# Kernel tuning notes

Hardware: AMD Instinct MI355X
Metric: run time of the kernel (lower is better)

## Reference

```python
import jax, jax.numpy as jnp
import numpy as np
from jax import lax

M = 4194304      # total ray samples
N_RAYS = 16384   # number of rays
INTERVAL = 0.5
ALPHA_INIT = 1e-6


def setup_inputs() -> dict:
    key = jax.random.key(0)
    k1, k2, k3 = jax.random.split(key, 3)
    density = jax.random.normal(k1, (M,), dtype=jnp.float32)
    rgb_raw = jax.random.normal(k2, (M, 3), dtype=jnp.float32)
    # act_shift buffer: log(1/(1-alpha_init) - 1)
    shift = jnp.full((1,), np.log(1.0 / (1.0 - ALPHA_INIT) - 1.0), dtype=jnp.float32)
    ray_id = jnp.sort(jax.random.randint(k3, (M,), 0, N_RAYS, dtype=jnp.int32))
    return {"density": density, "rgb_raw": rgb_raw, "shift": shift,
            "ray_id": ray_id, "N": N_RAYS}


def _seg_comb(a, b):
    # associative operator for segmented product scan: (prod, reset_flag)
    pa, fa = a
    pb, fb = b
    return jnp.where(fb, pb, pa * pb), fa | fb


def reference(density, rgb_raw, shift, ray_id, N):
    # Raw2Alpha: alpha = 1 - exp(-softplus(density + shift) * interval)
    s = jax.nn.softplus(density + shift[0]) * INTERVAL   # [M], >= 0
    alpha = -jnp.expm1(-s)                                # 1 - exp(-s), stable
    om = jnp.exp(-s)                                      # 1 - alpha, exact

    # Alphas2Weights: per-ray transmittance scan over variable-length segments.
    first = jnp.concatenate([jnp.ones((1,), bool), ray_id[1:] != ray_id[:-1]])
    # inclusive segmented cumprod of (1 - alpha)
    Tin, _ = lax.associative_scan(_seg_comb, (om, first))
    # exclusive transmittance: T_i = prod of (1-alpha_j) for j earlier in same ray
    T = jnp.where(first, 1.0, jnp.concatenate([jnp.ones((1,), om.dtype), Tin[:-1]]))
    weights = alpha * T                                   # [M]
    # leftover transmittance per ray (1 for rays with no samples)
    alphainv_last = jax.ops.segment_prod(om, ray_id, num_segments=N)  # [N]

    # alpha compositing of colors against a white background
    rgb = jax.nn.sigmoid(rgb_raw)                          # [M,3]
    rgb_marched = (jax.ops.segment_sum(weights[:, None] * rgb, ray_id, num_segments=N)
                   + alphainv_last[:, None])               # [N,3]
    return rgb_marched
```

## Files before the change

### kernel.cpp

```cpp
#include <hip/hip_runtime.h>
#include <math.h>


__device__ __forceinline__ float sigm(float x) {
    return __builtin_amdgcn_rcpf(1.0f + __expf(-x));
}

template <int Ctrl, int RowMask>
__device__ __forceinline__ float dpp_mul(float x) {
    const int s = __builtin_amdgcn_update_dpp(
        __float_as_int(1.0f), __float_as_int(x), Ctrl, RowMask, 0xf, false);
    return x * __int_as_float(s);
}
template <int Ctrl, int RowMask>
__device__ __forceinline__ float dpp_add(float x) {
    const int s = __builtin_amdgcn_update_dpp(
        __float_as_int(0.0f), __float_as_int(x), Ctrl, RowMask, 0xf, false);
    return x + __int_as_float(s);
}

__device__ __forceinline__ float wave_cumprod(float p) {
    p = dpp_mul<0x111, 0xf>(p);
    p = dpp_mul<0x112, 0xf>(p);
    p = dpp_mul<0x114, 0xf>(p);
    p = dpp_mul<0x118, 0xf>(p);
    p = dpp_mul<0x142, 0xa>(p);
    p = dpp_mul<0x143, 0xc>(p);
    return p;
}
__device__ __forceinline__ float wave_cumsum(float a) {
    a = dpp_add<0x111, 0xf>(a);
    a = dpp_add<0x112, 0xf>(a);
    a = dpp_add<0x114, 0xf>(a);
    a = dpp_add<0x118, 0xf>(a);
    a = dpp_add<0x142, 0xa>(a);
    a = dpp_add<0x143, 0xc>(a);
    return a;
}
__device__ __forceinline__ float lane63(float x) {
    return __int_as_float(__builtin_amdgcn_readlane(__float_as_int(x), 63));
}

__global__ __launch_bounds__(256) void seg_starts_kernel(
    const int* __restrict__ ray_id, int* __restrict__ starts, int M, int N)
{
    const int i4 = (blockIdx.x * 256 + threadIdx.x) * 4;
    if (i4 >= M) return;

    if (i4 + 3 < M) {
        const int4 v = *(const int4*)(ray_id + i4);
        const int prev = (i4 == 0) ? -1 : ray_id[i4 - 1];
        for (int r = prev + 1; r <= v.x; ++r) starts[r] = i4 + 0;
        for (int r = v.x + 1; r <= v.y; ++r) starts[r] = i4 + 1;
        for (int r = v.y + 1; r <= v.z; ++r) starts[r] = i4 + 2;
        for (int r = v.z + 1; r <= v.w; ++r) starts[r] = i4 + 3;
        if (i4 + 4 == M) {
            for (int r = v.w + 1; r <= N; ++r) starts[r] = M;
        }
    } else {
        int prev = (i4 == 0) ? -1 : ray_id[i4 - 1];
        for (int k = 0; k < 4 && i4 + k < M; ++k) {
            const int cur = ray_id[i4 + k];
            for (int r = prev + 1; r <= cur; ++r) starts[r] = i4 + k;
            prev = cur;
            if (i4 + k == M - 1)
                for (int r = cur + 1; r <= N; ++r) starts[r] = M;
        }
    }
}

__global__ __launch_bounds__(256) void voxel_march_kernel(
    const float* __restrict__ density,
    const float* __restrict__ rgb_raw,
    const float* __restrict__ shift,
    const int*   __restrict__ starts,
    float* __restrict__ out,
    int M, int N)
{
    const int lane = threadIdx.x & 63;
    const int wave = threadIdx.x >> 6;
    const int ray  = blockIdx.x * 4 + wave;
    if (ray >= N) return;

    const float sh = shift[0];
    const int begin = starts[ray];
    const int end   = starts[ray + 1];

    float carry = 1.0f;
    float acc0 = 0.0f, acc1 = 0.0f, acc2 = 0.0f;

    for (int base = (begin & ~3); base < end; base += 256) {
        const int b4 = base + 4 * lane;
        const int ba = min(b4, M - 4);

        const float4 dd = *(const float4*)(density + ba);
        const float4* rp = (const float4*)(rgb_raw + 3 * ba);
        const float4 c0 = rp[0], c1 = rp[1], c2 = rp[2];

        const bool v0 = (b4 + 0 >= begin) & (b4 + 0 < end);
        const bool v1 = (b4 + 1 >= begin) & (b4 + 1 < end);
        const bool v2 = (b4 + 2 >= begin) & (b4 + 2 < end);
        const bool v3 = (b4 + 3 >= begin) & (b4 + 3 < end);
        const float d0 = v0 ? dd.x : -1e30f;
        const float d1 = v1 ? dd.y : -1e30f;
        const float d2 = v2 ? dd.z : -1e30f;
        const float d3 = v3 ? dd.w : -1e30f;

        const float om0 = __builtin_amdgcn_rsqf(1.0f + __expf(d0 + sh));
        const float om1 = __builtin_amdgcn_rsqf(1.0f + __expf(d1 + sh));
        const float om2 = __builtin_amdgcn_rsqf(1.0f + __expf(d2 + sh));
        const float om3 = __builtin_amdgcn_rsqf(1.0f + __expf(d3 + sh));
        const float al0 = 1.0f - om0, al1 = 1.0f - om1;
        const float al2 = 1.0f - om2, al3 = 1.0f - om3;

        const float p = wave_cumprod((om0 * om1) * (om2 * om3));

        const float excl = __int_as_float(__builtin_amdgcn_update_dpp(
            __float_as_int(1.0f), __float_as_int(p), 0x138, 0xf, 0xf, false));

        float t = carry * excl;
        const float w0 = al0 * t; t *= om0;
        const float w1 = al1 * t; t *= om1;
        const float w2 = al2 * t; t *= om2;
        const float w3 = al3 * t;

        acc0 += w0 * sigm(c0.x) + w1 * sigm(c0.w) + w2 * sigm(c1.z) + w3 * sigm(c2.y);
        acc1 += w0 * sigm(c0.y) + w1 * sigm(c1.x) + w2 * sigm(c1.w) + w3 * sigm(c2.z);
        acc2 += w0 * sigm(c0.z) + w1 * sigm(c1.y) + w2 * sigm(c2.x) + w3 * sigm(c2.w);

        carry *= lane63(p);
    }

    const float tot0 = lane63(wave_cumsum(acc0));
    const float tot1 = lane63(wave_cumsum(acc1));
    const float tot2 = lane63(wave_cumsum(acc2));

    if (lane == 0) {
        out[3 * ray + 0] = tot0 + carry;
        out[3 * ray + 1] = tot1 + carry;
        out[3 * ray + 2] = tot2 + carry;
    }
}

extern "C" void kernel_launch(void* const* d_in, const int* in_sizes, int n_in,
                              void* d_out, int out_size, void* d_ws, size_t ws_size,
                              hipStream_t stream)
{
    const float* density = (const float*)d_in[0];
    const float* rgb_raw = (const float*)d_in[1];
    const float* shift   = (const float*)d_in[2];
    const int*   ray_id  = (const int*)d_in[3];
    float* out = (float*)d_out;

    const int M = in_sizes[0];
    const int N = out_size / 3;

    int* starts = (int*)d_ws;
    const int t1 = (M + 3) / 4;
    seg_starts_kernel<<<(t1 + 255) / 256, 256, 0, stream>>>(ray_id, starts, M, N);

    const int rays_per_block = 4;
    const int blocks = (N + rays_per_block - 1) / rays_per_block;
    voxel_march_kernel<<<blocks, 256, 0, stream>>>(density, rgb_raw, shift,
                                                   starts, out, M, N);
}
```

Before: 111.1 us.

## Replace per-ray marching with dense chunked segmented scan plus stitch pass

```diff
diff --git a/kernel.cpp b/kernel.cpp
--- a/kernel.cpp
+++ b/kernel.cpp
@@ -2,144 +2,198 @@
 #include <math.h>
 
 
+#define CHUNK 256
+
 __device__ __forceinline__ float sigm(float x) {
     return __builtin_amdgcn_rcpf(1.0f + __expf(-x));
 }
 
 template <int Ctrl, int RowMask>
-__device__ __forceinline__ float dpp_mul(float x) {
-    const int s = __builtin_amdgcn_update_dpp(
-        __float_as_int(1.0f), __float_as_int(x), Ctrl, RowMask, 0xf, false);
-    return x * __int_as_float(s);
+__device__ __forceinline__ float dpp_movf(float x, float old) {
+    return __int_as_float(__builtin_amdgcn_update_dpp(
+        __float_as_int(old), __float_as_int(x), Ctrl, RowMask, 0xf, false));
 }
 template <int Ctrl, int RowMask>
-__device__ __forceinline__ float dpp_add(float x) {
-    const int s = __builtin_amdgcn_update_dpp(
-        __float_as_int(0.0f), __float_as_int(x), Ctrl, RowMask, 0xf, false);
-    return x + __int_as_float(s);
-}
-
-__device__ __forceinline__ float wave_cumprod(float p) {
-    p = dpp_mul<0x111, 0xf>(p);
-    p = dpp_mul<0x112, 0xf>(p);
-    p = dpp_mul<0x114, 0xf>(p);
-    p = dpp_mul<0x118, 0xf>(p);
-    p = dpp_mul<0x142, 0xa>(p);
-    p = dpp_mul<0x143, 0xc>(p);
-    return p;
-}
-__device__ __forceinline__ float wave_cumsum(float a) {
-    a = dpp_add<0x111, 0xf>(a);
-    a = dpp_add<0x112, 0xf>(a);
-    a = dpp_add<0x114, 0xf>(a);
-    a = dpp_add<0x118, 0xf>(a);
-    a = dpp_add<0x142, 0xa>(a);
-    a = dpp_add<0x143, 0xc>(a);
-    return a;
-}
-__device__ __forceinline__ float lane63(float x) {
-    return __int_as_float(__builtin_amdgcn_readlane(__float_as_int(x), 63));
-}
-
-__global__ __launch_bounds__(256) void seg_starts_kernel(
-    const int* __restrict__ ray_id, int* __restrict__ starts, int M, int N)
-{
-    const int i4 = (blockIdx.x * 256 + threadIdx.x) * 4;
-    if (i4 >= M) return;
-
-    if (i4 + 3 < M) {
-        const int4 v = *(const int4*)(ray_id + i4);
-        const int prev = (i4 == 0) ? -1 : ray_id[i4 - 1];
-        for (int r = prev + 1; r <= v.x; ++r) starts[r] = i4 + 0;
-        for (int r = v.x + 1; r <= v.y; ++r) starts[r] = i4 + 1;
-        for (int r = v.y + 1; r <= v.z; ++r) starts[r] = i4 + 2;
-        for (int r = v.z + 1; r <= v.w; ++r) starts[r] = i4 + 3;
-        if (i4 + 4 == M) {
-            for (int r = v.w + 1; r <= N; ++r) starts[r] = M;
-        }
-    } else {
-        int prev = (i4 == 0) ? -1 : ray_id[i4 - 1];
-        for (int k = 0; k < 4 && i4 + k < M; ++k) {
-            const int cur = ray_id[i4 + k];
-            for (int r = prev + 1; r <= cur; ++r) starts[r] = i4 + k;
-            prev = cur;
-            if (i4 + k == M - 1)
-                for (int r = cur + 1; r <= N; ++r) starts[r] = M;
-        }
-    }
-}
-
-__global__ __launch_bounds__(256) void voxel_march_kernel(
+__device__ __forceinline__ int dpp_movi(int x, int old) {
+    return __builtin_amdgcn_update_dpp(old, x, Ctrl, RowMask, 0xf, false);
+}
+
+struct Seg { float p, s0, s1, s2; int f; };
+
+template <int Ctrl, int RowMask>
+__device__ __forceinline__ void seg_step(Seg& a) {
+    const float pp = dpp_movf<Ctrl, RowMask>(a.p, 1.0f);
+    const float t0 = dpp_movf<Ctrl, RowMask>(a.s0, 0.0f);
+    const float t1 = dpp_movf<Ctrl, RowMask>(a.s1, 0.0f);
+    const float t2 = dpp_movf<Ctrl, RowMask>(a.s2, 0.0f);
+    const int   ff = dpp_movi<Ctrl, RowMask>(a.f, 0);
+    const bool cut = (a.f != 0);
+    const float pa = cut ? 1.0f : pp;
+    a.s0 = fmaf(pa, a.s0, cut ? 0.0f : t0);
+    a.s1 = fmaf(pa, a.s1, cut ? 0.0f : t1);
+    a.s2 = fmaf(pa, a.s2, cut ? 0.0f : t2);
+    a.p  = pa * a.p;
+    a.f  = a.f | ff;
+}
+
+__global__ __launch_bounds__(256) void march_dense_kernel(
     const float* __restrict__ density,
     const float* __restrict__ rgb_raw,
     const float* __restrict__ shift,
-    const int*   __restrict__ starts,
+    const int*   __restrict__ ray_id,
     float* __restrict__ out,
-    int M, int N)
+    int2*   __restrict__ ids,
+    float4* __restrict__ head,
+    float4* __restrict__ tail,
+    int C)
 {
     const int lane = threadIdx.x & 63;
     const int wave = threadIdx.x >> 6;
-    const int ray  = blockIdx.x * 4 + wave;
-    if (ray >= N) return;
+    const int c    = blockIdx.x * 4 + wave;
+    if (c >= C) return;
+    const int base = c * CHUNK + 4 * lane;
 
     const float sh = shift[0];
-    const int begin = starts[ray];
-    const int end   = starts[ray + 1];
-
-    float carry = 1.0f;
-    float acc0 = 0.0f, acc1 = 0.0f, acc2 = 0.0f;
-
-    for (int base = (begin & ~3); base < end; base += 256) {
-        const int b4 = base + 4 * lane;
-        const int ba = min(b4, M - 4);
-
-        const float4 dd = *(const float4*)(density + ba);
-        const float4* rp = (const float4*)(rgb_raw + 3 * ba);
-        const float4 c0 = rp[0], c1 = rp[1], c2 = rp[2];
-
-        const bool v0 = (b4 + 0 >= begin) & (b4 + 0 < end);
-        const bool v1 = (b4 + 1 >= begin) & (b4 + 1 < end);
-        const bool v2 = (b4 + 2 >= begin) & (b4 + 2 < end);
-        const bool v3 = (b4 + 3 >= begin) & (b4 + 3 < end);
-        const float d0 = v0 ? dd.x : -1e30f;
-        const float d1 = v1 ? dd.y : -1e30f;
-        const float d2 = v2 ? dd.z : -1e30f;
-        const float d3 = v3 ? dd.w : -1e30f;
-
-        const float om0 = __builtin_amdgcn_rsqf(1.0f + __expf(d0 + sh));
-        const float om1 = __builtin_amdgcn_rsqf(1.0f + __expf(d1 + sh));
-        const float om2 = __builtin_amdgcn_rsqf(1.0f + __expf(d2 + sh));
-        const float om3 = __builtin_amdgcn_rsqf(1.0f + __expf(d3 + sh));
-        const float al0 = 1.0f - om0, al1 = 1.0f - om1;
-        const float al2 = 1.0f - om2, al3 = 1.0f - om3;
-
-        const float p = wave_cumprod((om0 * om1) * (om2 * om3));
-
-        const float excl = __int_as_float(__builtin_amdgcn_update_dpp(
-            __float_as_int(1.0f), __float_as_int(p), 0x138, 0xf, 0xf, false));
-
-        float t = carry * excl;
-        const float w0 = al0 * t; t *= om0;
-        const float w1 = al1 * t; t *= om1;
-        const float w2 = al2 * t; t *= om2;
-        const float w3 = al3 * t;
-
-        acc0 += w0 * sigm(c0.x) + w1 * sigm(c0.w) + w2 * sigm(c1.z) + w3 * sigm(c2.y);
-        acc1 += w0 * sigm(c0.y) + w1 * sigm(c1.x) + w2 * sigm(c1.w) + w3 * sigm(c2.z);
-        acc2 += w0 * sigm(c0.z) + w1 * sigm(c1.y) + w2 * sigm(c2.x) + w3 * sigm(c2.w);
-
-        carry *= lane63(p);
+
+    const int4   id4 = *(const int4*)(ray_id + base);
+    const float4 dd  = *(const float4*)(density + base);
+    const float4* rp = (const float4*)(rgb_raw + 3 * base);
+    const float4 c0 = rp[0], c1 = rp[1], c2 = rp[2];
+
+    const int  pid = dpp_movi<0x138, 0xf>(id4.w, 0);
+    const bool f0 = (lane != 0) && (id4.x != pid);
+    const bool f1 = (id4.y != id4.x);
+    const bool f2 = (id4.z != id4.y);
+    const bool f3 = (id4.w != id4.z);
+
+    const float om0 = __builtin_amdgcn_rsqf(1.0f + __expf(dd.x + sh));
+    const float om1 = __builtin_amdgcn_rsqf(1.0f + __expf(dd.y + sh));
+    const float om2 = __builtin_amdgcn_rsqf(1.0f + __expf(dd.z + sh));
+    const float om3 = __builtin_amdgcn_rsqf(1.0f + __expf(dd.w + sh));
+    const float al0 = 1.0f - om0, al1 = 1.0f - om1;
+    const float al2 = 1.0f - om2, al3 = 1.0f - om3;
+
+    const float g00 = sigm(c0.x), g01 = sigm(c0.y), g02 = sigm(c0.z);
+    const float g10 = sigm(c0.w), g11 = sigm(c1.x), g12 = sigm(c1.y);
+    const float g20 = sigm(c1.z), g21 = sigm(c1.w), g22 = sigm(c2.x);
+    const float g30 = sigm(c2.y), g31 = sigm(c2.z), g32 = sigm(c2.w);
+
+    Seg a; a.p = 1.0f; a.s0 = 0.0f; a.s1 = 0.0f; a.s2 = 0.0f; a.f = 0;
+#define P1(fk, alk, omk, ga, gb, gc)                                          \
+    if (fk) { a.p = 1.0f; a.s0 = 0.0f; a.s1 = 0.0f; a.s2 = 0.0f; a.f = 1; }   \
+    { const float t = a.p * alk;                                              \
+      a.s0 = fmaf(t, ga, a.s0); a.s1 = fmaf(t, gb, a.s1);                     \
+      a.s2 = fmaf(t, gc, a.s2); a.p *= omk; }
+    P1(f0, al0, om0, g00, g01, g02)
+    P1(f1, al1, om1, g10, g11, g12)
+    P1(f2, al2, om2, g20, g21, g22)
+    P1(f3, al3, om3, g30, g31, g32)
+#undef P1
+
+    seg_step<0x111, 0xf>(a);
+    seg_step<0x112, 0xf>(a);
+    seg_step<0x114, 0xf>(a);
+    seg_step<0x118, 0xf>(a);
+    seg_step<0x142, 0xa>(a);
+    seg_step<0x143, 0xc>(a);
+
+    const float pe  = dpp_movf<0x138, 0xf>(a.p, 1.0f);
+    const float se0 = dpp_movf<0x138, 0xf>(a.s0, 0.0f);
+    const float se1 = dpp_movf<0x138, 0xf>(a.s1, 0.0f);
+    const float se2 = dpp_movf<0x138, 0xf>(a.s2, 0.0f);
+    const int   fe  = dpp_movi<0x138, 0xf>(a.f, 0);
+
+    float T = pe, r0 = se0, r1 = se1, r2 = se2;
+    bool sb = (fe != 0);
+    int prev = pid;
+#define P2(fk, idk, alk, omk, ga, gb, gc)                                     \
+    if (fk) {                                                                 \
+        if (sb) { float* o = out + 3 * prev;                                  \
+                  o[0] = r0 + T; o[1] = r1 + T; o[2] = r2 + T; }              \
+        else    { head[c] = make_float4(r0, r1, r2, T); }                     \
+        for (int rr = prev + 1; rr < idk; ++rr) {                             \
+            float* o = out + 3 * rr; o[0] = 1.0f; o[1] = 1.0f; o[2] = 1.0f; } \
+        T = 1.0f; r0 = 0.0f; r1 = 0.0f; r2 = 0.0f; sb = true;                 \
+    }                                                                         \
+    { const float w = T * alk;                                                \
+      r0 = fmaf(w, ga, r0); r1 = fmaf(w, gb, r1); r2 = fmaf(w, gc, r2);       \
+      T *= omk; prev = idk; }
+    P2(f0, id4.x, al0, om0, g00, g01, g02)
+    P2(f1, id4.y, al1, om1, g10, g11, g12)
+    P2(f2, id4.z, al2, om2, g20, g21, g22)
+    P2(f3, id4.w, al3, om3, g30, g31, g32)
+#undef P2
+
+    if (lane == 63) tail[c] = make_float4(r0, r1, r2, T);
+    const int lastid = __builtin_amdgcn_readlane(id4.w, 63);
+    if (lane == 0) ids[c] = make_int2(id4.x, lastid);
+}
+
+__global__ __launch_bounds__(256) void stitch_kernel(
+    const int2*   __restrict__ ids,
+    const float4* __restrict__ head,
+    const float4* __restrict__ tail,
+    float* __restrict__ out,
+    int C, int N)
+{
+    const int b = blockIdx.x * 256 + threadIdx.x;
+    if (b > C) return;
+
+    if (b == 0) {
+        const int rc = ids[0].x;
+        for (int rr = 0; rr < rc; ++rr) {
+            float* o = out + 3 * rr; o[0] = 1.0f; o[1] = 1.0f; o[2] = 1.0f;
+        }
+        if (ids[0].y != rc) {
+            const float4 h = head[0];
+            float* o = out + 3 * rc;
+            o[0] = h.x + h.w; o[1] = h.y + h.w; o[2] = h.z + h.w;
+        }
+        return;
     }
 
-    const float tot0 = lane63(wave_cumsum(acc0));
-    const float tot1 = lane63(wave_cumsum(acc1));
-    const float tot2 = lane63(wave_cumsum(acc2));
-
-    if (lane == 0) {
-        out[3 * ray + 0] = tot0 + carry;
-        out[3 * ray + 1] = tot1 + carry;
-        out[3 * ray + 2] = tot2 + carry;
+    float cs0, cs1, cs2, cp;
+    int r, j;
+    if (b == C) {
+        r = ids[C - 1].y;
+        cs0 = cs1 = cs2 = 0.0f; cp = 1.0f; j = C - 1;
+        for (int rr = r + 1; rr < N; ++rr) {
+            float* o = out + 3 * rr; o[0] = 1.0f; o[1] = 1.0f; o[2] = 1.0f;
+        }
+    } else {
+        const int rp_ = ids[b - 1].y, rc_ = ids[b].x;
+        if (rp_ == rc_) {
+            r = rc_;
+            if (ids[b].y == r) return;
+            const float4 h = head[b];
+            cs0 = h.x; cs1 = h.y; cs2 = h.z; cp = h.w; j = b - 1;
+        } else {
+            r = rp_;
+            cs0 = cs1 = cs2 = 0.0f; cp = 1.0f; j = b - 1;
+            for (int rr = rp_ + 1; rr < rc_; ++rr) {
+                float* o = out + 3 * rr; o[0] = 1.0f; o[1] = 1.0f; o[2] = 1.0f;
+            }
+            if (ids[b].y != rc_) {
+                const float4 h = head[b];
+                float* o = out + 3 * rc_;
+                o[0] = h.x + h.w; o[1] = h.y + h.w; o[2] = h.z + h.w;
+            }
+        }
     }
+
+    while (j >= 0 && ids[j].y == r) {
+        const float4 t = tail[j];
+        cs0 = fmaf(t.w, cs0, t.x);
+        cs1 = fmaf(t.w, cs1, t.y);
+        cs2 = fmaf(t.w, cs2, t.z);
+        cp *= t.w;
+        if (ids[j].x != r) break;
+        if (j == 0) break;
+        if (ids[j - 1].y != r) break;
+        j--;
+    }
+    float* o = out + 3 * r;
+    o[0] = cs0 + cp; o[1] = cs1 + cp; o[2] = cs2 + cp;
 }
 
 extern "C" void kernel_launch(void* const* d_in, const int* in_sizes, int n_in,
@@ -154,13 +208,14 @@
 
     const int M = in_sizes[0];
     const int N = out_size / 3;
-
-    int* starts = (int*)d_ws;
-    const int t1 = (M + 3) / 4;
-    seg_starts_kernel<<<(t1 + 255) / 256, 256, 0, stream>>>(ray_id, starts, M, N);
-
-    const int rays_per_block = 4;
-    const int blocks = (N + rays_per_block - 1) / rays_per_block;
-    voxel_march_kernel<<<blocks, 256, 0, stream>>>(density, rgb_raw, shift,
-                                                   starts, out, M, N);
-}
+    const int C = M / CHUNK;
+
+    int2*   ids  = (int2*)d_ws;
+    float4* head = (float4*)((char*)d_ws + (((size_t)C * sizeof(int2) + 255) & ~(size_t)255));
+    float4* tail = head + C;
+
+    const int blocks = (C + 3) / 4;
+    march_dense_kernel<<<blocks, 256, 0, stream>>>(density, rgb_raw, shift,
+                                                   ray_id, out, ids, head, tail, C);
+    stitch_kernel<<<(C + 1 + 255) / 256, 256, 0, stream>>>(ids, head, tail, out, C, N);
+}
```

Measured after the change: 109.0 us (median of 2 runs). About the same (-1.9%).
